# Kernel tuning notes

Hardware: AMD Instinct MI355X
Metric: run time of the kernel (lower is better)

Reference implementation:

```python
import jax, jax.numpy as jnp
import numpy as np

B, S, D, H, E = 2, 2048, 1024, 4096, 8


def setup_inputs() -> dict:
    key = jax.random.key(0)
    ks = jax.random.split(key, 8)
    sc = lambda *shape: 0.02
    x = jax.random.normal(ks[0], (B, S, D), dtype=jnp.float32)
    gate_w = jax.random.normal(ks[1], (D, E), dtype=jnp.float32) * 0.02
    gate_b = jnp.zeros((E,), dtype=jnp.float32)
    w1 = jax.random.normal(ks[2], (E, D, H), dtype=jnp.float32) * 0.02
    b1 = jnp.zeros((E, H), dtype=jnp.float32)
    w2 = jax.random.normal(ks[3], (E, H, D), dtype=jnp.float32) * 0.02
    b2 = jnp.zeros((E, D), dtype=jnp.float32)
    return {"x": x, "gate_w": gate_w, "gate_b": gate_b,
            "w1": w1, "b1": b1, "w2": w2, "b2": b2}


def reference(x, gate_w, gate_b, w1, b1, w2, b2):
    b, s, d = x.shape
    e = w1.shape[0]
    xf = x.reshape(-1, d)                       # [N, D]
    scores = xf @ gate_w + gate_b               # [N, E]
    # original does topk(k=2) but only uses topk_indices[:, 0] == argmax
    sel = jnp.argmax(scores, axis=-1)           # [N]
    out = jnp.zeros_like(xf)
    for ei in range(e):                         # small fixed expert loop
        h = jax.nn.gelu(xf @ w1[ei] + b1[ei], approximate=False)
        y = h @ w2[ei] + b2[ei]
        out = out + jnp.where((sel == ei)[:, None], y, jnp.zeros((), x.dtype))
    out = out.reshape(b, s, d)
    l_aux = jnp.zeros((), dtype=x.dtype)
    return out, l_aux
```

## Files before the change

kernel.cpp:

```cpp
#include <hip/hip_runtime.h>
#include <math.h>

#define NTOK 4096
#define DDIM 1024
#define HDIM 4096
#define NEXP 8
#define BK 64
#define T0MAX 40
#define T1MAX 72

typedef float f32x4 __attribute__((ext_vector_type(4)));
typedef __bf16 bf16x8 __attribute__((ext_vector_type(8)));
typedef const __attribute__((address_space(1))) void gas_t;
typedef __attribute__((address_space(3))) void las_t;

__device__ __forceinline__ unsigned short f2bf(float f) {
    union { float f; unsigned u; } v; v.f = f;
    unsigned u = v.u;
    return (unsigned short)((u + 0x7fffu + ((u >> 16) & 1u)) >> 16);
}

__device__ __forceinline__ float gelu_f(float v) {
    return 0.5f * v * (1.0f + erff(v * 0.70710678118654752f));
}

__global__ void k_gate(const float* __restrict__ x, const float* __restrict__ gw,
                       const float* __restrict__ gb, unsigned short* __restrict__ xb,
                       int* __restrict__ sel, int* __restrict__ counts) {
    const int wid = threadIdx.x >> 6, lane = threadIdx.x & 63;
    const int tok = blockIdx.x * 4 + wid;
    const float* xr = x + (long)tok * DDIM;
    unsigned short* xbr = xb + (long)tok * DDIM;
    float s[NEXP];
#pragma unroll
    for (int e = 0; e < NEXP; ++e) s[e] = 0.f;
    for (int it = 0; it < DDIM / 64; ++it) {
        const int kk = it * 64 + lane;
        const float xv = xr[kk];
        xbr[kk] = f2bf(xv);
        const float4* g4 = (const float4*)(gw + (long)kk * NEXP);
        const float4 g0 = g4[0], g1 = g4[1];
        s[0] += xv * g0.x; s[1] += xv * g0.y; s[2] += xv * g0.z; s[3] += xv * g0.w;
        s[4] += xv * g1.x; s[5] += xv * g1.y; s[6] += xv * g1.z; s[7] += xv * g1.w;
    }
#pragma unroll
    for (int e = 0; e < NEXP; ++e)
        for (int off = 32; off > 0; off >>= 1)
            s[e] += __shfl_down(s[e], off);
    if (lane == 0) {
        float best = s[0] + gb[0]; int bi = 0;
#pragma unroll
        for (int e = 1; e < NEXP; ++e) {
            const float v = s[e] + gb[e];
            if (v > best) { best = v; bi = e; }
        }
        sel[tok] = bi;
        atomicAdd(&counts[bi], 1);
    }
}

__global__ void k_fill(const int* __restrict__ sel, const int* __restrict__ counts,
                       int* __restrict__ cur, int* __restrict__ offs,
                       int* __restrict__ list, int* __restrict__ t0,
                       int* __restrict__ t1, float* __restrict__ laux) {
    const int t = blockIdx.x * blockDim.x + threadIdx.x;
    if (t < NTOK) {
        const int e = sel[t];
        int off_e = 0;
#pragma unroll
        for (int j = 0; j < NEXP; ++j) off_e += (j < e) ? counts[j] : 0;
        list[off_e + atomicAdd(&cur[e], 1)] = t;
    }
    if (t == 0) {
        int o = 0;
        for (int e = 0; e < NEXP; ++e) { offs[e] = o; o += counts[e]; }
        offs[NEXP] = o;
        int i0 = 0;
        for (int e = 0; e < NEXP; ++e)
            for (int m = 0; m < counts[e]; m += 128) t0[i0++] = (e << 16) | m;
        while (i0 < T0MAX) t0[i0++] = -1;
        int i1 = 0;
        for (int e = 0; e < NEXP; ++e)
            for (int m = 0; m < counts[e]; m += 64) t1[i1++] = (e << 16) | m;
        while (i1 < T1MAX) t1[i1++] = -1;
        laux[0] = 0.f;
    }
}

template<int K, int NC>
__global__ __launch_bounds__(256) void k_cvt_w(const float* __restrict__ W,
                                               unsigned short* __restrict__ Wt) {
    __shared__ unsigned short T[64 * 68];
    const int ktiles = K / 64;
    const int e  = blockIdx.y / ktiles;
    const int k0 = (blockIdx.y % ktiles) * 64;
    const int n0 = blockIdx.x * 64;
    const float* src = W + (long)e * K * NC + (long)k0 * NC + n0;
    const int tid = threadIdx.x;
#pragma unroll
    for (int i = 0; i < 4; ++i) {
        const int idx = tid + i * 256;
        const int k = idx >> 4, c4 = (idx & 15) * 4;
        const float4 v = *(const float4*)(src + (long)k * NC + c4);
        T[(c4 + 0) * 68 + k] = f2bf(v.x);
        T[(c4 + 1) * 68 + k] = f2bf(v.y);
        T[(c4 + 2) * 68 + k] = f2bf(v.z);
        T[(c4 + 3) * 68 + k] = f2bf(v.w);
    }
    __syncthreads();
    unsigned short* dst = Wt + (long)e * NC * K + (long)n0 * K + k0;
#pragma unroll
    for (int i = 0; i < 2; ++i) {
        const int idx = tid + i * 256;
        const int n = idx >> 3, c8 = (idx & 7) * 8;
        *(ushort4*)(dst + (long)n * K + c8)     = *(const ushort4*)&T[n * 68 + c8];
        *(ushort4*)(dst + (long)n * K + c8 + 4) = *(const ushort4*)&T[n * 68 + c8 + 4];
    }
}

template<int MODE, int BM_, int BN_>
__global__ __launch_bounds__(256) void k_gemm(
        const unsigned short* __restrict__ Ain,
        const unsigned short* __restrict__ Wt,
        const float* __restrict__ bias,
        unsigned short* __restrict__ Hout, float* __restrict__ Yout,
        const int* __restrict__ counts, const int* __restrict__ offs,
        const int* __restrict__ list, const int* __restrict__ ttab) {
    static_assert(BM_ % 32 == 0 && BN_ % 32 == 0, "tile");
    constexpr int K    = (MODE == 0) ? DDIM : HDIM;
    constexpr int NC   = (MODE == 0) ? HDIM : DDIM;
    constexpr int NT   = K / BK;
    constexpr int FM   = BM_ / 32;
    constexpr int FN   = BN_ / 32;
    constexpr int LA   = BM_ / 32;
    constexpr int LB   = BN_ / 32;
    constexpr int HALF = BM_ * 64 + BN_ * 64;
    constexpr int EP   = 136;
    constexpr int SH_SZ = (2 * HALF > BM_ * EP) ? 2 * HALF : BM_ * EP;

    const int code = ttab[blockIdx.y];
    if (code < 0) return;
    const int e  = code >> 16;
    const int m0 = code & 0xFFFF;
    const int cnt  = counts[e];
    const int base = offs[e];
    const int n0   = blockIdx.x * BN_;

    __shared__ __align__(16) unsigned short sh[SH_SZ];

    const int tid  = threadIdx.x;
    const int lane = tid & 63, wid = tid >> 6;
    const int lr = lane >> 3, lc = lane & 7;
    const int sb = (lc * 16) ^ (lr << 4);

    const unsigned short* pA[LA];
#pragma unroll
    for (int i = 0; i < LA; ++i) {
        const int r = wid * (BM_ / 4) + i * 8 + lr;
        int rr = m0 + r; if (rr >= cnt) rr = cnt - 1;
        const long grow = (MODE == 0) ? (long)list[base + rr] : (long)(base + rr);
        pA[i] = (const unsigned short*)((const char*)(Ain + grow * K) + sb);
    }
    const unsigned short* We = Wt + (long)e * NC * K;
    const unsigned short* pB[LB];
#pragma unroll
    for (int i = 0; i < LB; ++i) {
        const int r = wid * (BN_ / 4) + i * 8 + lr;
        pB[i] = (const unsigned short*)((const char*)(We + (long)(n0 + r) * K) + sb);
    }

    const int wm = (wid >> 1) * (BM_ / 2);
    const int wn = (wid & 1) * (BN_ / 2);
    const int hk = 16 * (lane >> 4);

#define STAGE(t) do { if ((t) < NT) {                                                    \
    unsigned short* Ad = sh + ((t) & 1) * HALF + (wid * (BM_ / 4)) * 64;                 \
    unsigned short* Bd = sh + ((t) & 1) * HALF + BM_ * 64 + (wid * (BN_ / 4)) * 64;      \
    _Pragma("unroll") for (int i = 0; i < LA; ++i)                                       \
        __builtin_amdgcn_global_load_lds((gas_t*)(pA[i] + (t) * 64),                     \
            (las_t*)(Ad + i * 512), 16, 0, 0);                                           \
    _Pragma("unroll") for (int i = 0; i < LB; ++i)                                       \
        __builtin_amdgcn_global_load_lds((gas_t*)(pB[i] + (t) * 64),                     \
            (las_t*)(Bd + i * 512), 16, 0, 0); } } while (0)

    const f32x4 zero4 = {0.f, 0.f, 0.f, 0.f};
    f32x4 acc[FM][FN];
#pragma unroll
    for (int i = 0; i < FM; ++i)
#pragma unroll
        for (int j = 0; j < FN; ++j) acc[i][j] = zero4;

    STAGE(0);
    STAGE(1);

    for (int t = 0; t < NT; ++t) {
        const unsigned short* Ab = sh + (t & 1) * HALF;
        const unsigned short* Bb = Ab + BM_ * 64;
        if (t + 1 < NT) { asm volatile("s_waitcnt vmcnt(%0)" :: "n"(LA + LB) : "memory"); }
        else            { asm volatile("s_waitcnt vmcnt(0)" ::: "memory"); }
        __builtin_amdgcn_sched_barrier(0);
        __builtin_amdgcn_s_barrier();
        __builtin_amdgcn_sched_barrier(0);
#pragma unroll
        for (int kk = 0; kk < BK; kk += 32) {
            bf16x8 a[FM], b[FN];
#pragma unroll
            for (int mf = 0; mf < FM; ++mf) {
                const int r  = wm + mf * 16 + (lane & 15);
                const int kb = (2 * kk + hk) ^ ((r & 7) << 4);
                a[mf] = *(const bf16x8*)((const char*)Ab + r * 128 + kb);
            }
#pragma unroll
            for (int nf = 0; nf < FN; ++nf) {
                const int cc = wn + nf * 16 + (lane & 15);
                const int kb = (2 * kk + hk) ^ ((cc & 7) << 4);
                b[nf] = *(const bf16x8*)((const char*)Bb + cc * 128 + kb);
            }
            __builtin_amdgcn_s_setprio(1);
#pragma unroll
            for (int mf = 0; mf < FM; ++mf)
#pragma unroll
                for (int nf = 0; nf < FN; ++nf)
                    acc[mf][nf] = __builtin_amdgcn_mfma_f32_16x16x32_bf16(
                        a[mf], b[nf], acc[mf][nf], 0, 0, 0);
            __builtin_amdgcn_s_setprio(0);
        }
        __builtin_amdgcn_sched_barrier(0);
        __builtin_amdgcn_s_barrier();
        __builtin_amdgcn_sched_barrier(0);
        STAGE(t + 2);
    }
#undef STAGE

    if constexpr (MODE == 0) {
#pragma unroll
        for (int nf = 0; nf < FN; ++nf) {
            const int cl = wn + nf * 16 + (lane & 15);
            const float bv = bias[(long)e * NC + n0 + cl];
#pragma unroll
            for (int mf = 0; mf < FM; ++mf) {
#pragma unroll
                for (int ri = 0; ri < 4; ++ri) {
                    const int rl = wm + mf * 16 + (lane >> 4) * 4 + ri;
                    sh[rl * EP + cl] = f2bf(gelu_f(acc[mf][nf][ri] + bv));
                }
            }
        }
        __syncthreads();
        const int row = tid >> 1, ch = (tid & 1) * 64;
        if (m0 + row < cnt) {
            char* dst = (char*)(Hout + (long)(base + m0 + row) * HDIM + n0 + ch);
            const char* srcp = (const char*)sh + row * (EP * 2) + ch * 2;
#pragma unroll
            for (int j = 0; j < 4; ++j) {
                const int4 v0 = *(const int4*)(srcp + j * 32);
                const int4 v1 = *(const int4*)(srcp + j * 32 + 16);
                *(int4*)(dst + j * 32)      = v0;
                *(int4*)(dst + j * 32 + 16) = v1;
            }
        }
    } else {
#pragma unroll
        for (int nf = 0; nf < FN; ++nf) {
            const int coln = n0 + wn + nf * 16 + (lane & 15);
            const float bv = bias[(long)e * NC + coln];
#pragma unroll
            for (int mf = 0; mf < FM; ++mf) {
                const int rb = m0 + wm + mf * 16 + (lane >> 4) * 4;
#pragma unroll
                for (int ri = 0; ri < 4; ++ri) {
                    const int row = rb + ri;
                    if (row < cnt)
                        Yout[(long)list[base + row] * DDIM + coln] = acc[mf][nf][ri] + bv;
                }
            }
        }
    }
}

extern "C" void kernel_launch(void* const* d_in, const int* in_sizes, int n_in,
                              void* d_out, int out_size, void* d_ws, size_t ws_size,
                              hipStream_t stream) {
    const float* x      = (const float*)d_in[0];
    const float* gate_w = (const float*)d_in[1];
    const float* gate_b = (const float*)d_in[2];
    const float* w1     = (const float*)d_in[3];
    const float* b1     = (const float*)d_in[4];
    const float* w2     = (const float*)d_in[5];
    const float* b2     = (const float*)d_in[6];
    float* out = (float*)d_out;

    char* ws = (char*)d_ws;
    int* counts  = (int*)(ws);
    int* cur     = (int*)(ws + 128);
    int* offs    = (int*)(ws + 256);
    int* t0      = (int*)(ws + 512);
    int* t1      = (int*)(ws + 768);
    int* sel     = (int*)(ws + 4096);
    int* list    = (int*)(ws + 20480);
    unsigned short* xb  = (unsigned short*)(ws + 65536);
    unsigned short* Hws = (unsigned short*)(ws + 65536 + 8388608);
    unsigned short* Wtb = (unsigned short*)(ws + 65536 + 8388608 + 33554432);
    const size_t WS_NEEDED = 65536 + 8388608 + 33554432 + 67108864;
    if (ws_size < WS_NEEDED) return;

    hipMemsetAsync(ws, 0, 256, stream);
    k_gate<<<NTOK / 4, 256, 0, stream>>>(x, gate_w, gate_b, xb, sel, counts);
    k_fill<<<(NTOK + 255) / 256, 256, 0, stream>>>(sel, counts, cur, offs, list, t0, t1,
                                                   out + (long)NTOK * DDIM);

    k_cvt_w<DDIM, HDIM><<<dim3(HDIM / 64, NEXP * (DDIM / 64)), 256, 0, stream>>>(w1, Wtb);
    k_gemm<0, 128, 128><<<dim3(HDIM / 128, T0MAX), 256, 0, stream>>>(
        xb, Wtb, b1, Hws, nullptr, counts, offs, list, t0);

    k_cvt_w<HDIM, DDIM><<<dim3(DDIM / 64, NEXP * (HDIM / 64)), 256, 0, stream>>>(w2, Wtb);
    k_gemm<1, 64, 64><<<dim3(DDIM / 64, T1MAX), 256, 0, stream>>>(
        Hws, Wtb, b2, nullptr, out, counts, offs, list, t1);
}
```

Before: 285.2 us.

## Overlap W2 bf16 conversion with first expert GEMM in one fused launch

The first grouped GEMM launch gets extra blocks that convert and transpose W2 to bf16, so the conversion runs alongside the GEMM instead of as a separate launch afterwards. This needs a separate workspace buffer for W2t, and the code falls back to the old sequential path when the workspace is too small. The gate kernel also switches to float4 loads of x and vectorized bf16 stores. The fused path depends on the harness giving a larger workspace, and the extra blocks compete with GEMM blocks for compute units.

```diff
diff --git a/kernel.cpp b/kernel.cpp
--- a/kernel.cpp
+++ b/kernel.cpp
@@ -8,6 +8,8 @@
 #define BK 64
 #define T0MAX 40
 #define T1MAX 72
+#define NG0 ((HDIM / 128) * T0MAX)
+#define NCVT2 ((DDIM / 64) * (NEXP * (HDIM / 64)))
 
 typedef float f32x4 __attribute__((ext_vector_type(4)));
 typedef __bf16 bf16x8 __attribute__((ext_vector_type(8)));
@@ -29,19 +31,24 @@
                        int* __restrict__ sel, int* __restrict__ counts) {
     const int wid = threadIdx.x >> 6, lane = threadIdx.x & 63;
     const int tok = blockIdx.x * 4 + wid;
-    const float* xr = x + (long)tok * DDIM;
+    const float4* xr4 = (const float4*)(x + (long)tok * DDIM);
     unsigned short* xbr = xb + (long)tok * DDIM;
     float s[NEXP];
 #pragma unroll
     for (int e = 0; e < NEXP; ++e) s[e] = 0.f;
-    for (int it = 0; it < DDIM / 64; ++it) {
-        const int kk = it * 64 + lane;
-        const float xv = xr[kk];
-        xbr[kk] = f2bf(xv);
-        const float4* g4 = (const float4*)(gw + (long)kk * NEXP);
-        const float4 g0 = g4[0], g1 = g4[1];
-        s[0] += xv * g0.x; s[1] += xv * g0.y; s[2] += xv * g0.z; s[3] += xv * g0.w;
-        s[4] += xv * g1.x; s[5] += xv * g1.y; s[6] += xv * g1.z; s[7] += xv * g1.w;
+#pragma unroll
+    for (int it = 0; it < DDIM / 256; ++it) {
+        const int q = it * 64 + lane;
+        const float4 xv = xr4[q];
+        *(ushort4*)(xbr + q * 4) = make_ushort4(f2bf(xv.x), f2bf(xv.y), f2bf(xv.z), f2bf(xv.w));
+#pragma unroll
+        for (int j = 0; j < 4; ++j) {
+            const float xs = (j == 0) ? xv.x : (j == 1) ? xv.y : (j == 2) ? xv.z : xv.w;
+            const float4* g4 = (const float4*)(gw + (long)(q * 4 + j) * NEXP);
+            const float4 g0 = g4[0], g1 = g4[1];
+            s[0] += xs * g0.x; s[1] += xs * g0.y; s[2] += xs * g0.z; s[3] += xs * g0.w;
+            s[4] += xs * g1.x; s[5] += xs * g1.y; s[6] += xs * g1.z; s[7] += xs * g1.w;
+        }
     }
 #pragma unroll
     for (int e = 0; e < NEXP; ++e)
@@ -88,13 +95,13 @@
 }
 
 template<int K, int NC>
-__global__ __launch_bounds__(256) void k_cvt_w(const float* __restrict__ W,
-                                               unsigned short* __restrict__ Wt) {
-    __shared__ unsigned short T[64 * 68];
-    const int ktiles = K / 64;
-    const int e  = blockIdx.y / ktiles;
-    const int k0 = (blockIdx.y % ktiles) * 64;
-    const int n0 = blockIdx.x * 64;
+__device__ __forceinline__ void cvt_tile(const float* __restrict__ W,
+                                         unsigned short* __restrict__ Wt,
+                                         int bx, int by, unsigned short* T) {
+    constexpr int ktiles = K / 64;
+    const int e  = by / ktiles;
+    const int k0 = (by % ktiles) * 64;
+    const int n0 = bx * 64;
     const float* src = W + (long)e * K * NC + (long)k0 * NC + n0;
     const int tid = threadIdx.x;
 #pragma unroll
@@ -118,14 +125,22 @@
     }
 }
 
-template<int MODE, int BM_, int BN_>
+template<int K, int NC>
+__global__ __launch_bounds__(256) void k_cvt_w(const float* __restrict__ W,
+                                               unsigned short* __restrict__ Wt) {
+    __shared__ unsigned short T[64 * 68];
+    cvt_tile<K, NC>(W, Wt, blockIdx.x, blockIdx.y, T);
+}
+
+template<int MODE, int BM_, int BN_, bool FUSE>
 __global__ __launch_bounds__(256) void k_gemm(
         const unsigned short* __restrict__ Ain,
         const unsigned short* __restrict__ Wt,
         const float* __restrict__ bias,
         unsigned short* __restrict__ Hout, float* __restrict__ Yout,
         const int* __restrict__ counts, const int* __restrict__ offs,
-        const int* __restrict__ list, const int* __restrict__ ttab) {
+        const int* __restrict__ list, const int* __restrict__ ttab,
+        const float* __restrict__ Wcvt, unsigned short* __restrict__ Wtcvt) {
     static_assert(BM_ % 32 == 0 && BN_ % 32 == 0, "tile");
     constexpr int K    = (MODE == 0) ? DDIM : HDIM;
     constexpr int NC   = (MODE == 0) ? HDIM : DDIM;
@@ -138,15 +153,28 @@
     constexpr int EP   = 136;
     constexpr int SH_SZ = (2 * HALF > BM_ * EP) ? 2 * HALF : BM_ * EP;
 
-    const int code = ttab[blockIdx.y];
+    __shared__ __align__(16) unsigned short sh[SH_SZ];
+
+    int bx, by;
+    if constexpr (FUSE) {
+        const int bid = blockIdx.x;
+        if (bid >= NG0) {
+            const int cv = bid - NG0;
+            cvt_tile<HDIM, DDIM>(Wcvt, Wtcvt, cv % (DDIM / 64), cv / (DDIM / 64), sh);
+            return;
+        }
+        bx = bid % (NC / BN_); by = bid / (NC / BN_);
+    } else {
+        bx = blockIdx.x; by = blockIdx.y;
+    }
+
+    const int code = ttab[by];
     if (code < 0) return;
     const int e  = code >> 16;
     const int m0 = code & 0xFFFF;
     const int cnt  = counts[e];
     const int base = offs[e];
-    const int n0   = blockIdx.x * BN_;
-
-    __shared__ __align__(16) unsigned short sh[SH_SZ];
+    const int n0   = bx * BN_;
 
     const int tid  = threadIdx.x;
     const int lane = tid & 63, wid = tid >> 6;
@@ -300,20 +328,30 @@
     int* list    = (int*)(ws + 20480);
     unsigned short* xb  = (unsigned short*)(ws + 65536);
     unsigned short* Hws = (unsigned short*)(ws + 65536 + 8388608);
-    unsigned short* Wtb = (unsigned short*)(ws + 65536 + 8388608 + 33554432);
-    const size_t WS_NEEDED = 65536 + 8388608 + 33554432 + 67108864;
-    if (ws_size < WS_NEEDED) return;
+    unsigned short* W1t = (unsigned short*)(ws + 65536 + 8388608 + 33554432);
+    unsigned short* W2s = W1t + (size_t)NEXP * HDIM * DDIM;
+    const size_t WS_SMALL = 65536 + 8388608 + 33554432 + 67108864;
+    const size_t WS_BIG   = WS_SMALL + 67108864;
+    if (ws_size < WS_SMALL) return;
+    const bool big = ws_size >= WS_BIG;
+    unsigned short* W2t = big ? W2s : W1t;
 
     hipMemsetAsync(ws, 0, 256, stream);
     k_gate<<<NTOK / 4, 256, 0, stream>>>(x, gate_w, gate_b, xb, sel, counts);
     k_fill<<<(NTOK + 255) / 256, 256, 0, stream>>>(sel, counts, cur, offs, list, t0, t1,
                                                    out + (long)NTOK * DDIM);
 
-    k_cvt_w<DDIM, HDIM><<<dim3(HDIM / 64, NEXP * (DDIM / 64)), 256, 0, stream>>>(w1, Wtb);
-    k_gemm<0, 128, 128><<<dim3(HDIM / 128, T0MAX), 256, 0, stream>>>(
-        xb, Wtb, b1, Hws, nullptr, counts, offs, list, t0);
-
-    k_cvt_w<HDIM, DDIM><<<dim3(DDIM / 64, NEXP * (HDIM / 64)), 256, 0, stream>>>(w2, Wtb);
-    k_gemm<1, 64, 64><<<dim3(DDIM / 64, T1MAX), 256, 0, stream>>>(
-        Hws, Wtb, b2, nullptr, out, counts, offs, list, t1);
-}
+    k_cvt_w<DDIM, HDIM><<<dim3(HDIM / 64, NEXP * (DDIM / 64)), 256, 0, stream>>>(w1, W1t);
+
+    if (big) {
+        k_gemm<0, 128, 128, true><<<NG0 + NCVT2, 256, 0, stream>>>(
+            xb, W1t, b1, Hws, nullptr, counts, offs, list, t0, w2, W2t);
+    } else {
+        k_gemm<0, 128, 128, false><<<dim3(HDIM / 128, T0MAX), 256, 0, stream>>>(
+            xb, W1t, b1, Hws, nullptr, counts, offs, list, t0, nullptr, nullptr);
+        k_cvt_w<HDIM, DDIM><<<dim3(DDIM / 64, NEXP * (HDIM / 64)), 256, 0, stream>>>(w2, W2t);
+    }
+
+    k_gemm<1, 64, 64, false><<<dim3(DDIM / 64, T1MAX), 256, 0, stream>>>(
+        Hws, W2t, b2, nullptr, out, counts, offs, list, t1, nullptr, nullptr);
+}
```

Result: faster. 279.2 us (-2.1%).
